# Performance work log

Hardware: AMD Instinct MI355X
Metric: run time of the kernel (lower is better)

## Reference

```python
import jax, jax.numpy as jnp
import numpy as np

B, T, F = 8192, 30, 16
H1, H2 = 64, 32


def _lstm(x, Wih, Whh, b):
    """PyTorch-convention LSTM (gate order i,f,g,o). x: [B,T,I] -> (ys [B,T,H], hT [B,H])."""
    H = Whh.shape[1]
    h0 = jnp.zeros((x.shape[0], H), x.dtype)

    def step(carry, xt):
        h, c = carry
        z = xt @ Wih.T + h @ Whh.T + b  # [B,4H]
        i, f, g, o = jnp.split(z, 4, axis=-1)
        c = jax.nn.sigmoid(f) * c + jax.nn.sigmoid(i) * jnp.tanh(g)
        h = jax.nn.sigmoid(o) * jnp.tanh(c)
        return (h, c), h

    (hT, _), ys = jax.lax.scan(step, (h0, h0), jnp.swapaxes(x, 0, 1))
    return jnp.swapaxes(ys, 0, 1), hT


def setup_inputs() -> dict:
    key = jax.random.key(0)
    ks = jax.random.split(key, 16)
    s = 0.1  # small init scale for numerical sanity
    return {
        "x": jax.random.normal(ks[0], (B, T, F), jnp.float32),
        "Wih1": jax.random.normal(ks[1], (4 * H1, F), jnp.float32) * s,
        "Whh1": jax.random.normal(ks[2], (4 * H1, H1), jnp.float32) * s,
        "b1": jax.random.normal(ks[3], (4 * H1,), jnp.float32) * s,
        "Wih2": jax.random.normal(ks[4], (4 * H2, H1), jnp.float32) * s,
        "Whh2": jax.random.normal(ks[5], (4 * H2, H2), jnp.float32) * s,
        "b2": jax.random.normal(ks[6], (4 * H2,), jnp.float32) * s,
        "Wih3": jax.random.normal(ks[7], (4 * H2, H2), jnp.float32) * s,
        "Whh3": jax.random.normal(ks[8], (4 * H2, H2), jnp.float32) * s,
        "b3": jax.random.normal(ks[9], (4 * H2,), jnp.float32) * s,
        "Wih4": jax.random.normal(ks[10], (4 * H1, H2), jnp.float32) * s,
        "Whh4": jax.random.normal(ks[11], (4 * H1, H1), jnp.float32) * s,
        "b4": jax.random.normal(ks[12], (4 * H1,), jnp.float32) * s,
        "Wout": jax.random.normal(ks[13], (F, H1), jnp.float32) * s,
        "bout": jax.random.normal(ks[14], (F,), jnp.float32) * s,
    }


def reference(x, Wih1, Whh1, b1, Wih2, Whh2, b2, Wih3, Whh3, b3, Wih4, Whh4, b4, Wout, bout):
    ys1, _ = _lstm(x, Wih1, Whh1, b1)          # encoder LSTM(64)
    _, latent = _lstm(ys1, Wih2, Whh2, b2)      # encoder LSTM(32) -> final hidden [B,32]
    repeated = jnp.broadcast_to(latent[:, None, :], (latent.shape[0], T, latent.shape[1]))
    ys3, _ = _lstm(repeated, Wih3, Whh3, b3)    # decoder LSTM(32)
    ys4, _ = _lstm(ys3, Wih4, Whh4, b4)         # decoder LSTM(64)
    return ys4 @ Wout.T + bout                  # [B,T,F]
```

## Files before the change

### kernel.cpp

```cpp
#include <hip/hip_runtime.h>


#define TT 30
#define FF 16
#define NT 768

typedef unsigned short u16t;
typedef __attribute__((ext_vector_type(8))) short short8;
typedef __attribute__((ext_vector_type(4))) short short4v;
typedef __attribute__((ext_vector_type(4))) float floatx4;

#define MFMA(a, b, c) __builtin_amdgcn_mfma_f32_16x16x32_bf16(a, b, c, 0, 0, 0)

#if __has_builtin(__builtin_amdgcn_exp2f)
#define EXP2(x) __builtin_amdgcn_exp2f(x)
#else
#define EXP2(x) exp2f(x)
#endif

template <int P> struct IC { static constexpr int v = P; };

__device__ __forceinline__ float rcpf(float v) { return __builtin_amdgcn_rcpf(v); }
__device__ __forceinline__ u16t f2bf(float f) {
  unsigned int u = __float_as_uint(f);
  u = (u + 0x7FFFu + ((u >> 16) & 1u)) >> 16;
  return (u16t)u;
}
__device__ __forceinline__ unsigned int pkbf(float a, float b) {
  unsigned int r;
  asm("v_cvt_pk_bf16_f32 %0, %1, %2" : "=v"(r) : "v"(a), "v"(b));
  return r;
}
__device__ __forceinline__ void barLDS() {
  asm volatile("s_waitcnt lgkmcnt(0)" ::: "memory");
  __builtin_amdgcn_s_barrier();
}
__device__ __forceinline__ short8 ldFragS(const float* p, float s) {
  const float4 lo = *(const float4*)p;
  const float4 hi = *(const float4*)(p + 4);
  short8 r;
  r[0] = (short)f2bf(lo.x * s); r[1] = (short)f2bf(lo.y * s);
  r[2] = (short)f2bf(lo.z * s); r[3] = (short)f2bf(lo.w * s);
  r[4] = (short)f2bf(hi.x * s); r[5] = (short)f2bf(hi.y * s);
  r[6] = (short)f2bf(hi.z * s); r[7] = (short)f2bf(hi.w * s);
  return r;
}
__device__ __forceinline__ float cellUp(const floatx4 acc, float& c) {
  float ei = EXP2(-acc[0]);
  float ef = EXP2(-acc[1]);
  float eg = EXP2(-acc[2]);
  float eo = EXP2(-acc[3]);
  float pig = (1.f + ei) * (1.f + eg);
  float pf  = 1.f + ef;
  float num = c * pig + (1.f - eg) * pf;
  c = num * rcpf(pf * pig);
  float ec = EXP2(-2.885390082f * c);
  return (1.f - ec) * rcpf((1.f + eo) * (1.f + ec));
}

__global__ __launch_bounds__(NT, 3) void lstm_ae_mfma11(
    const float* __restrict__ x,
    const float* __restrict__ Wih1, const float* __restrict__ Whh1, const float* __restrict__ b1,
    const float* __restrict__ Wih2, const float* __restrict__ Whh2, const float* __restrict__ b2,
    const float* __restrict__ Wih3, const float* __restrict__ Whh3, const float* __restrict__ b3,
    const float* __restrict__ Wih4, const float* __restrict__ Whh4, const float* __restrict__ b4,
    const float* __restrict__ Wout, const float* __restrict__ bout,
    float* __restrict__ out)
{
  __shared__ __align__(16) u16t xAll[32 * 968];
  __shared__ __align__(16) u16t aB[32 * 264];

  const int t = threadIdx.x;
  const int w = t >> 6, lane = t & 63;
  const int q = lane >> 4, n = lane & 15;
  const int q8 = q * 8;
  const int bBase = blockIdx.x * 32;
  const int nlo = n >> 2, ngt = n & 3;
  const int r0 = n * 264, r1 = (n + 16) * 264;
  const int x0 = n * 968, x1 = (n + 16) * 968;
  const bool isZ1 = (w < 8);
  const int u = w & 3;

  const float L1 = 1.442695041f, L2 = 2.885390082f;
  const float sA = (ngt == 2) ? L2 : L1;

  for (int i = t; i < 32 * 264; i += NT) aB[i] = 0;
  {
    const float* xb = x + (size_t)bBase * (TT * FF);
    for (int i4 = t; i4 < 3840; i4 += NT) {
      int e = i4 * 4;
      int b = e / 480, r = e - b * 480;
      int stp = r >> 4, f = r & 15;
      float4 v = *(const float4*)&xb[e];
      short4v s4 = { (short)f2bf(v.x), (short)f2bf(v.y), (short)f2bf(v.z), (short)f2bf(v.w) };
      *(short4v*)&xAll[b * 968 + stp * 32 + f] = s4;
    }
    for (int i = t; i < 15360; i += NT) {
      int b = i / 480, r = i - b * 480;
      int stp = r >> 4, f = r & 15;
      xAll[b * 968 + stp * 32 + 16 + f] = 0;
    }
  }
  const short8 z8 = { 0, 0, 0, 0, 0, 0, 0, 0 };
  short8 wAf[2][3]; floatx4 biasA[2];
  if (isZ1) {
#pragma unroll
    for (int tt = 0; tt < 2; ++tt) {
      int T = w + 8 * tt;
      int row = ngt * 64 + T * 4 + nlo;
      wAf[tt][0] = z8;
      if (q < 2) wAf[tt][0] = ldFragS(&Wih1[row * 16 + q8], sA);
      wAf[tt][1] = ldFragS(&Whh1[row * 64 + q8], sA);
      wAf[tt][2] = ldFragS(&Whh1[row * 64 + 32 + q8], sA);
#pragma unroll
      for (int r = 0; r < 4; ++r) biasA[tt][r] = b1[r * 64 + T * 4 + q] * (r == 2 ? L2 : L1);
    }
  } else {
#pragma unroll
    for (int tt = 0; tt < 2; ++tt) {
      int T = 2 * u + tt;
      int row = ngt * 32 + T * 4 + nlo;
      wAf[tt][0] = ldFragS(&Wih2[row * 64 + q8], sA);
      wAf[tt][1] = ldFragS(&Wih2[row * 64 + 32 + q8], sA);
      wAf[tt][2] = ldFragS(&Whh2[row * 32 + q8], sA);
#pragma unroll
      for (int r = 0; r < 4; ++r) biasA[tt][r] = b2[r * 32 + T * 4 + q] * (r == 2 ? L2 : L1);
    }
  }
  __syncthreads();

  float cA[2][2] = {{0.f, 0.f}, {0.f, 0.f}};
  short8 bxN[2];
  float h0v[2], h1v[2];

  if (isZ1) {
    const short8 bx0 = *(const short8*)&xAll[x0 + q8];
    const short8 bx1 = *(const short8*)&xAll[x1 + q8];
#pragma unroll
    for (int tt = 0; tt < 2; ++tt) {
      floatx4 a0 = biasA[tt], a1 = biasA[tt];
      a0 = MFMA(wAf[tt][0], bx0, a0);
      a1 = MFMA(wAf[tt][0], bx1, a1);
      h0v[tt] = cellUp(a0, cA[0][tt]);
      h1v[tt] = cellUp(a1, cA[1][tt]);
    }
    unsigned int pk0 = pkbf(h0v[0], h0v[1]);
    unsigned int pk1 = pkbf(h1v[0], h1v[1]);
    aB[r0 + w * 4 + q] = (u16t)pk0;
    aB[r0 + (w + 8) * 4 + q] = (u16t)(pk0 >> 16);
    aB[r1 + w * 4 + q] = (u16t)pk1;
    aB[r1 + (w + 8) * 4 + q] = (u16t)(pk1 >> 16);
    bxN[0] = *(const short8*)&xAll[x0 + 32 + q8];
    bxN[1] = *(const short8*)&xAll[x1 + 32 + q8];
  }
  barLDS();

  auto stepA = [&](int st, auto pc) {
    constexpr int p = decltype(pc)::v;
    const short8 h1a0 = *(const short8*)&aB[r0 + p * 64 + q8];
    const short8 h1b0 = *(const short8*)&aB[r0 + p * 64 + 32 + q8];
    const short8 h1a1 = *(const short8*)&aB[r1 + p * 64 + q8];
    const short8 h1b1 = *(const short8*)&aB[r1 + p * 64 + 32 + q8];
    if (isZ1) {
#pragma unroll
      for (int tt = 0; tt < 2; ++tt) {
        floatx4 a0 = biasA[tt], a1 = biasA[tt];
        a0 = MFMA(wAf[tt][0], bxN[0], a0);
        a1 = MFMA(wAf[tt][0], bxN[1], a1);
        a0 = MFMA(wAf[tt][1], h1a0, a0);
        a1 = MFMA(wAf[tt][1], h1a1, a1);
        a0 = MFMA(wAf[tt][2], h1b0, a0);
        a1 = MFMA(wAf[tt][2], h1b1, a1);
        h0v[tt] = cellUp(a0, cA[0][tt]);
        h1v[tt] = cellUp(a1, cA[1][tt]);
      }
      unsigned int pk0 = pkbf(h0v[0], h0v[1]);
      unsigned int pk1 = pkbf(h1v[0], h1v[1]);
      aB[r0 + (1 - p) * 64 + w * 4 + q] = (u16t)pk0;
      aB[r0 + (1 - p) * 64 + (w + 8) * 4 + q] = (u16t)(pk0 >> 16);
      aB[r1 + (1 - p) * 64 + w * 4 + q] = (u16t)pk1;
      aB[r1 + (1 - p) * 64 + (w + 8) * 4 + q] = (u16t)(pk1 >> 16);
      const int nx = (st + 2 < TT) ? st + 2 : TT - 1;
      bxN[0] = *(const short8*)&xAll[x0 + nx * 32 + q8];
      bxN[1] = *(const short8*)&xAll[x1 + nx * 32 + q8];
    } else {
      const short8 h20 = *(const short8*)&aB[r0 + 128 + (1 - p) * 32 + q8];
      const short8 h21 = *(const short8*)&aB[r1 + 128 + (1 - p) * 32 + q8];
#pragma unroll
      for (int tt = 0; tt < 2; ++tt) {
        floatx4 a0 = biasA[tt], a1 = biasA[tt];
        a0 = MFMA(wAf[tt][0], h1a0, a0);
        a1 = MFMA(wAf[tt][0], h1a1, a1);
        a0 = MFMA(wAf[tt][1], h1b0, a0);
        a1 = MFMA(wAf[tt][1], h1b1, a1);
        a0 = MFMA(wAf[tt][2], h20, a0);
        a1 = MFMA(wAf[tt][2], h21, a1);
        h0v[tt] = cellUp(a0, cA[0][tt]);
        h1v[tt] = cellUp(a1, cA[1][tt]);
      }
      unsigned int pk0 = pkbf(h0v[0], h0v[1]);
      unsigned int pk1 = pkbf(h1v[0], h1v[1]);
      aB[r0 + 128 + p * 32 + (2 * u) * 4 + q] = (u16t)pk0;
      aB[r0 + 128 + p * 32 + (2 * u + 1) * 4 + q] = (u16t)(pk0 >> 16);
      aB[r1 + 128 + p * 32 + (2 * u) * 4 + q] = (u16t)pk1;
      aB[r1 + 128 + p * 32 + (2 * u + 1) * 4 + q] = (u16t)(pk1 >> 16);
    }
    barLDS();
  };
  for (int st = 0; st < 28; st += 2) { stepA(st, IC<0>{}); stepA(st + 1, IC<1>{}); }
  stepA(28, IC<0>{});
  if (!isZ1) {
    const short8 h1a0 = *(const short8*)&aB[r0 + 64 + q8];
    const short8 h1b0 = *(const short8*)&aB[r0 + 96 + q8];
    const short8 h1a1 = *(const short8*)&aB[r1 + 64 + q8];
    const short8 h1b1 = *(const short8*)&aB[r1 + 96 + q8];
    const short8 h20  = *(const short8*)&aB[r0 + 128 + q8];
    const short8 h21  = *(const short8*)&aB[r1 + 128 + q8];
#pragma unroll
    for (int tt = 0; tt < 2; ++tt) {
      floatx4 a0 = biasA[tt], a1 = biasA[tt];
      a0 = MFMA(wAf[tt][0], h1a0, a0);
      a1 = MFMA(wAf[tt][0], h1a1, a1);
      a0 = MFMA(wAf[tt][1], h1b0, a0);
      a1 = MFMA(wAf[tt][1], h1b1, a1);
      a0 = MFMA(wAf[tt][2], h20, a0);
      a1 = MFMA(wAf[tt][2], h21, a1);
      h0v[tt] = cellUp(a0, cA[0][tt]);
      h1v[tt] = cellUp(a1, cA[1][tt]);
    }
    unsigned int pk0 = pkbf(h0v[0], h0v[1]);
    unsigned int pk1 = pkbf(h1v[0], h1v[1]);
    aB[r0 + 160 + (2 * u) * 4 + q] = (u16t)pk0;
    aB[r0 + 160 + (2 * u + 1) * 4 + q] = (u16t)(pk0 >> 16);
    aB[r1 + 160 + (2 * u) * 4 + q] = (u16t)pk1;
    aB[r1 + 160 + (2 * u + 1) * 4 + q] = (u16t)(pk1 >> 16);
  }
  __syncthreads();

  short8 wBf[2][3]; floatx4 biasB[2];
  short8 wof[2]; floatx4 biasO;
  short8 w3h[2]; floatx4 acc3c[2][2];
  if (isZ1) {
#pragma unroll
    for (int tt = 0; tt < 2; ++tt) {
      int T = w + 8 * tt;
      int row = ngt * 64 + T * 4 + nlo;
      wBf[tt][0] = ldFragS(&Wih4[row * 32 + q8], sA);
      wBf[tt][1] = ldFragS(&Whh4[row * 64 + q8], sA);
      wBf[tt][2] = ldFragS(&Whh4[row * 64 + 32 + q8], sA);
#pragma unroll
      for (int r = 0; r < 4; ++r) biasB[tt][r] = b4[r * 64 + T * 4 + q] * (r == 2 ? L2 : L1);
    }
    wof[0] = ldFragS(&Wout[n * 64 + q8], 1.f);
    wof[1] = ldFragS(&Wout[n * 64 + 32 + q8], 1.f);
    biasO = *(const floatx4*)&bout[q * 4];
  } else {
    const short8 blat0 = *(const short8*)&aB[r0 + 160 + q8];
    const short8 blat1 = *(const short8*)&aB[r1 + 160 + q8];
#pragma unroll
    for (int tt = 0; tt < 2; ++tt) {
      int T = 2 * u + tt;
      int row = ngt * 32 + T * 4 + nlo;
      const short8 w3i = ldFragS(&Wih3[row * 32 + q8], sA);
      w3h[tt] = ldFragS(&Whh3[row * 32 + q8], sA);
      floatx4 b3v;
#pragma unroll
      for (int r = 0; r < 4; ++r) b3v[r] = b3[r * 32 + T * 4 + q] * (r == 2 ? L2 : L1);
      acc3c[tt][0] = MFMA(w3i, blat0, b3v);
      acc3c[tt][1] = MFMA(w3i, blat1, b3v);
    }
  }
  for (int i = t; i < 2048; i += NT) aB[(i >> 6) * 264 + 64 + (i & 63)] = 0;
  __syncthreads();

  float cB[2][2] = {{0.f, 0.f}, {0.f, 0.f}};

  if (!isZ1) {
#pragma unroll
    for (int tt = 0; tt < 2; ++tt) {
      h0v[tt] = cellUp(acc3c[tt][0], cB[0][tt]);
      h1v[tt] = cellUp(acc3c[tt][1], cB[1][tt]);
    }
    unsigned int pk0 = pkbf(h0v[0], h0v[1]);
    unsigned int pk1 = pkbf(h1v[0], h1v[1]);
    aB[r0 + 192 + (2 * u) * 4 + q] = (u16t)pk0;
    aB[r0 + 192 + (2 * u + 1) * 4 + q] = (u16t)(pk0 >> 16);
    aB[r1 + 192 + (2 * u) * 4 + q] = (u16t)pk1;
    aB[r1 + 192 + (2 * u + 1) * 4 + q] = (u16t)(pk1 >> 16);
  }
  barLDS();

  auto stepB = [&](int st, auto pc) {
    constexpr int p = decltype(pc)::v;
    const short8 h30 = *(const short8*)&aB[r0 + 192 + p * 32 + q8];
    const short8 h31 = *(const short8*)&aB[r1 + 192 + p * 32 + q8];
    if (isZ1) {
      const short8 h4a0 = *(const short8*)&aB[r0 + (1 - p) * 64 + q8];
      const short8 h4b0 = *(const short8*)&aB[r0 + (1 - p) * 64 + 32 + q8];
      const short8 h4a1 = *(const short8*)&aB[r1 + (1 - p) * 64 + q8];
      const short8 h4b1 = *(const short8*)&aB[r1 + (1 - p) * 64 + 32 + q8];
#pragma unroll
      for (int tt = 0; tt < 2; ++tt) {
        floatx4 a0 = biasB[tt], a1 = biasB[tt];
        a0 = MFMA(wBf[tt][0], h30, a0);
        a1 = MFMA(wBf[tt][0], h31, a1);
        a0 = MFMA(wBf[tt][1], h4a0, a0);
        a1 = MFMA(wBf[tt][1], h4a1, a1);
        a0 = MFMA(wBf[tt][2], h4b0, a0);
        a1 = MFMA(wBf[tt][2], h4b1, a1);
        h0v[tt] = cellUp(a0, cB[0][tt]);
        h1v[tt] = cellUp(a1, cB[1][tt]);
      }
      unsigned int pk0 = pkbf(h0v[0], h0v[1]);
      unsigned int pk1 = pkbf(h1v[0], h1v[1]);
      aB[r0 + p * 64 + w * 4 + q] = (u16t)pk0;
      aB[r0 + p * 64 + (w + 8) * 4 + q] = (u16t)(pk0 >> 16);
      aB[r1 + p * 64 + w * 4 + q] = (u16t)pk1;
      aB[r1 + p * 64 + (w + 8) * 4 + q] = (u16t)(pk1 >> 16);
      if (st > 0 && w == ((st - 1) & 7)) {
        floatx4 y0 = biasO, y1 = biasO;
        y0 = MFMA(wof[0], h4a0, y0);
        y1 = MFMA(wof[0], h4a1, y1);
        y0 = MFMA(wof[1], h4b0, y0);
        y1 = MFMA(wof[1], h4b1, y1);
        *(floatx4*)&out[((size_t)(bBase + n) * TT + (st - 1)) * FF + q * 4] = y0;
        *(floatx4*)&out[((size_t)(bBase + n + 16) * TT + (st - 1)) * FF + q * 4] = y1;
      }
    } else {
#pragma unroll
      for (int tt = 0; tt < 2; ++tt) {
        floatx4 a0 = MFMA(w3h[tt], h30, acc3c[tt][0]);
        floatx4 a1 = MFMA(w3h[tt], h31, acc3c[tt][1]);
        h0v[tt] = cellUp(a0, cB[0][tt]);
        h1v[tt] = cellUp(a1, cB[1][tt]);
      }
      unsigned int pk0 = pkbf(h0v[0], h0v[1]);
      unsigned int pk1 = pkbf(h1v[0], h1v[1]);
      aB[r0 + 192 + (1 - p) * 32 + (2 * u) * 4 + q] = (u16t)pk0;
      aB[r0 + 192 + (1 - p) * 32 + (2 * u + 1) * 4 + q] = (u16t)(pk0 >> 16);
      aB[r1 + 192 + (1 - p) * 32 + (2 * u) * 4 + q] = (u16t)pk1;
      aB[r1 + 192 + (1 - p) * 32 + (2 * u + 1) * 4 + q] = (u16t)(pk1 >> 16);
    }
    barLDS();
  };
  for (int st = 0; st < 28; st += 2) { stepB(st, IC<0>{}); stepB(st + 1, IC<1>{}); }
  stepB(28, IC<0>{});
  if (isZ1) {
    const short8 h30  = *(const short8*)&aB[r0 + 224 + q8];
    const short8 h31  = *(const short8*)&aB[r1 + 224 + q8];
    const short8 h4a0 = *(const short8*)&aB[r0 + q8];
    const short8 h4b0 = *(const short8*)&aB[r0 + 32 + q8];
    const short8 h4a1 = *(const short8*)&aB[r1 + q8];
    const short8 h4b1 = *(const short8*)&aB[r1 + 32 + q8];
#pragma unroll
    for (int tt = 0; tt < 2; ++tt) {
      floatx4 a0 = biasB[tt], a1 = biasB[tt];
      a0 = MFMA(wBf[tt][0], h30, a0);
      a1 = MFMA(wBf[tt][0], h31, a1);
      a0 = MFMA(wBf[tt][1], h4a0, a0);
      a1 = MFMA(wBf[tt][1], h4a1, a1);
      a0 = MFMA(wBf[tt][2], h4b0, a0);
      a1 = MFMA(wBf[tt][2], h4b1, a1);
      h0v[tt] = cellUp(a0, cB[0][tt]);
      h1v[tt] = cellUp(a1, cB[1][tt]);
    }
    unsigned int pk0 = pkbf(h0v[0], h0v[1]);
    unsigned int pk1 = pkbf(h1v[0], h1v[1]);
    aB[r0 + 64 + w * 4 + q] = (u16t)pk0;
    aB[r0 + 64 + (w + 8) * 4 + q] = (u16t)(pk0 >> 16);
    aB[r1 + 64 + w * 4 + q] = (u16t)pk1;
    aB[r1 + 64 + (w + 8) * 4 + q] = (u16t)(pk1 >> 16);
    if (w == 4) {
      floatx4 y0 = biasO, y1 = biasO;
      y0 = MFMA(wof[0], h4a0, y0);
      y1 = MFMA(wof[0], h4a1, y1);
      y0 = MFMA(wof[1], h4b0, y0);
      y1 = MFMA(wof[1], h4b1, y1);
      *(floatx4*)&out[((size_t)(bBase + n) * TT + 28) * FF + q * 4] = y0;
      *(floatx4*)&out[((size_t)(bBase + n + 16) * TT + 28) * FF + q * 4] = y1;
    }
  }
  barLDS();
  if (w == 5) {
    const short8 ba0 = *(const short8*)&aB[r0 + 64 + q8];
    const short8 bb0 = *(const short8*)&aB[r0 + 96 + q8];
    const short8 ba1 = *(const short8*)&aB[r1 + 64 + q8];
    const short8 bb1 = *(const short8*)&aB[r1 + 96 + q8];
    floatx4 y0 = biasO, y1 = biasO;
    y0 = MFMA(wof[0], ba0, y0);
    y1 = MFMA(wof[0], ba1, y1);
    y0 = MFMA(wof[1], bb0, y0);
    y1 = MFMA(wof[1], bb1, y1);
    *(floatx4*)&out[((size_t)(bBase + n) * TT + 29) * FF + q * 4] = y0;
    *(floatx4*)&out[((size_t)(bBase + n + 16) * TT + 29) * FF + q * 4] = y1;
  }
}

extern "C" void kernel_launch(void* const* d_in, const int* in_sizes, int n_in,
                              void* d_out, int out_size, void* d_ws, size_t ws_size,
                              hipStream_t stream) {
  const float* x    = (const float*)d_in[0];
  const float* Wih1 = (const float*)d_in[1];
  const float* Whh1 = (const float*)d_in[2];
  const float* b1   = (const float*)d_in[3];
  const float* Wih2 = (const float*)d_in[4];
  const float* Whh2 = (const float*)d_in[5];
  const float* b2   = (const float*)d_in[6];
  const float* Wih3 = (const float*)d_in[7];
  const float* Whh3 = (const float*)d_in[8];
  const float* b3   = (const float*)d_in[9];
  const float* Wih4 = (const float*)d_in[10];
  const float* Whh4 = (const float*)d_in[11];
  const float* b4   = (const float*)d_in[12];
  const float* Wout = (const float*)d_in[13];
  const float* bout = (const float*)d_in[14];
  float* out = (float*)d_out;

  const int B = in_sizes[0] / (TT * FF);
  dim3 grid(B / 32), block(NT);
  lstm_ae_mfma11<<<grid, block, 0, stream>>>(
      x, Wih1, Whh1, b1, Wih2, Whh2, b2, Wih3, Whh3, b3,
      Wih4, Whh4, b4, Wout, bout, out);
}
```

Measured before the change: 156.1 us.

## Move output projection to decoder-layer-3 warps and merge x zero-padding loop

```diff
diff --git a/kernel.cpp b/kernel.cpp
--- a/kernel.cpp
+++ b/kernel.cpp
@@ -58,7 +58,7 @@
   return (1.f - ec) * rcpf((1.f + eo) * (1.f + ec));
 }
 
-__global__ __launch_bounds__(NT, 3) void lstm_ae_mfma11(
+__global__ __launch_bounds__(NT, 3) void lstm_ae_mfma14(
     const float* __restrict__ x,
     const float* __restrict__ Wih1, const float* __restrict__ Whh1, const float* __restrict__ b1,
     const float* __restrict__ Wih2, const float* __restrict__ Whh2, const float* __restrict__ b2,
@@ -87,6 +87,7 @@
   for (int i = t; i < 32 * 264; i += NT) aB[i] = 0;
   {
     const float* xb = x + (size_t)bBase * (TT * FF);
+    const short4v z4v = { 0, 0, 0, 0 };
     for (int i4 = t; i4 < 3840; i4 += NT) {
       int e = i4 * 4;
       int b = e / 480, r = e - b * 480;
@@ -94,11 +95,7 @@
       float4 v = *(const float4*)&xb[e];
       short4v s4 = { (short)f2bf(v.x), (short)f2bf(v.y), (short)f2bf(v.z), (short)f2bf(v.w) };
       *(short4v*)&xAll[b * 968 + stp * 32 + f] = s4;
-    }
-    for (int i = t; i < 15360; i += NT) {
-      int b = i / 480, r = i - b * 480;
-      int stp = r >> 4, f = r & 15;
-      xAll[b * 968 + stp * 32 + 16 + f] = 0;
+      *(short4v*)&xAll[b * 968 + stp * 32 + 16 + f] = z4v;
     }
   }
   const short8 z8 = { 0, 0, 0, 0, 0, 0, 0, 0 };
@@ -251,9 +248,6 @@
 #pragma unroll
       for (int r = 0; r < 4; ++r) biasB[tt][r] = b4[r * 64 + T * 4 + q] * (r == 2 ? L2 : L1);
     }
-    wof[0] = ldFragS(&Wout[n * 64 + q8], 1.f);
-    wof[1] = ldFragS(&Wout[n * 64 + 32 + q8], 1.f);
-    biasO = *(const floatx4*)&bout[q * 4];
   } else {
     const short8 blat0 = *(const short8*)&aB[r0 + 160 + q8];
     const short8 blat1 = *(const short8*)&aB[r1 + 160 + q8];
@@ -269,6 +263,9 @@
       acc3c[tt][0] = MFMA(w3i, blat0, b3v);
       acc3c[tt][1] = MFMA(w3i, blat1, b3v);
     }
+    wof[0] = ldFragS(&Wout[n * 64 + q8], 1.f);
+    wof[1] = ldFragS(&Wout[n * 64 + 32 + q8], 1.f);
+    biasO = *(const floatx4*)&bout[q * 4];
   }
   for (int i = t; i < 2048; i += NT) aB[(i >> 6) * 264 + 64 + (i & 63)] = 0;
   __syncthreads();
@@ -317,16 +314,20 @@
       aB[r0 + p * 64 + (w + 8) * 4 + q] = (u16t)(pk0 >> 16);
       aB[r1 + p * 64 + w * 4 + q] = (u16t)pk1;
       aB[r1 + p * 64 + (w + 8) * 4 + q] = (u16t)(pk1 >> 16);
-      if (st > 0 && w == ((st - 1) & 7)) {
+    } else {
+      if (st > 0 && u == ((st - 1) & 3)) {
+        const short8 pa0 = *(const short8*)&aB[r0 + (1 - p) * 64 + q8];
+        const short8 pb0 = *(const short8*)&aB[r0 + (1 - p) * 64 + 32 + q8];
+        const short8 pa1 = *(const short8*)&aB[r1 + (1 - p) * 64 + q8];
+        const short8 pb1 = *(const short8*)&aB[r1 + (1 - p) * 64 + 32 + q8];
         floatx4 y0 = biasO, y1 = biasO;
-        y0 = MFMA(wof[0], h4a0, y0);
-        y1 = MFMA(wof[0], h4a1, y1);
-        y0 = MFMA(wof[1], h4b0, y0);
-        y1 = MFMA(wof[1], h4b1, y1);
+        y0 = MFMA(wof[0], pa0, y0);
+        y1 = MFMA(wof[0], pa1, y1);
+        y0 = MFMA(wof[1], pb0, y0);
+        y1 = MFMA(wof[1], pb1, y1);
         *(floatx4*)&out[((size_t)(bBase + n) * TT + (st - 1)) * FF + q * 4] = y0;
         *(floatx4*)&out[((size_t)(bBase + n + 16) * TT + (st - 1)) * FF + q * 4] = y1;
       }
-    } else {
 #pragma unroll
       for (int tt = 0; tt < 2; ++tt) {
         floatx4 a0 = MFMA(w3h[tt], h30, acc3c[tt][0]);
@@ -370,18 +371,21 @@
     aB[r0 + 64 + (w + 8) * 4 + q] = (u16t)(pk0 >> 16);
     aB[r1 + 64 + w * 4 + q] = (u16t)pk1;
     aB[r1 + 64 + (w + 8) * 4 + q] = (u16t)(pk1 >> 16);
-    if (w == 4) {
-      floatx4 y0 = biasO, y1 = biasO;
-      y0 = MFMA(wof[0], h4a0, y0);
-      y1 = MFMA(wof[0], h4a1, y1);
-      y0 = MFMA(wof[1], h4b0, y0);
-      y1 = MFMA(wof[1], h4b1, y1);
-      *(floatx4*)&out[((size_t)(bBase + n) * TT + 28) * FF + q * 4] = y0;
-      *(floatx4*)&out[((size_t)(bBase + n + 16) * TT + 28) * FF + q * 4] = y1;
-    }
+  } else if (u == 0) {
+    const short8 pa0 = *(const short8*)&aB[r0 + q8];
+    const short8 pb0 = *(const short8*)&aB[r0 + 32 + q8];
+    const short8 pa1 = *(const short8*)&aB[r1 + q8];
+    const short8 pb1 = *(const short8*)&aB[r1 + 32 + q8];
+    floatx4 y0 = biasO, y1 = biasO;
+    y0 = MFMA(wof[0], pa0, y0);
+    y1 = MFMA(wof[0], pa1, y1);
+    y0 = MFMA(wof[1], pb0, y0);
+    y1 = MFMA(wof[1], pb1, y1);
+    *(floatx4*)&out[((size_t)(bBase + n) * TT + 28) * FF + q * 4] = y0;
+    *(floatx4*)&out[((size_t)(bBase + n + 16) * TT + 28) * FF + q * 4] = y1;
   }
   barLDS();
-  if (w == 5) {
+  if (!isZ1 && u == 1) {
     const short8 ba0 = *(const short8*)&aB[r0 + 64 + q8];
     const short8 bb0 = *(const short8*)&aB[r0 + 96 + q8];
     const short8 ba1 = *(const short8*)&aB[r1 + 64 + q8];
@@ -418,7 +422,7 @@
 
   const int B = in_sizes[0] / (TT * FF);
   dim3 grid(B / 32), block(NT);
-  lstm_ae_mfma11<<<grid, block, 0, stream>>>(
+  lstm_ae_mfma14<<<grid, block, 0, stream>>>(
       x, Wih1, Whh1, b1, Wih2, Whh2, b2, Wih3, Whh3, b3,
       Wih4, Whh4, b4, Wout, bout, out);
 }
```

New measurement: 155.2 us. About the same (-0.6%).
